# Kernel tuning notes

Hardware: AMD Instinct MI355X
Metric: run time of the kernel (lower is better)

## Reference

```python
import jax, jax.numpy as jnp
import numpy as np

DIM = 256
WH, WW = 7, 7
N = WH * WW
HEADS = 8
HEAD_DIM = DIM // HEADS
SCALE = HEAD_DIM ** -0.5
B_ = 4096
NW = 64  # windows per image; B_ % NW == 0


def _relative_position_index():
    coords = np.stack(np.meshgrid(np.arange(WH), np.arange(WW), indexing='ij'))  # (2,Wh,Ww)
    flat = coords.reshape(2, -1)  # (2,N)
    rel = flat[:, :, None] - flat[:, None, :]  # (2,N,N)
    rel = rel.transpose(1, 2, 0)  # (N,N,2)
    rel = rel + np.array([WH - 1, WW - 1])
    rel = rel * np.array([2 * WW - 1, 1])
    return rel.sum(-1).astype(np.int32)  # (N,N)


def setup_inputs() -> dict:
    key = jax.random.key(0)
    ks = jax.random.split(key, 7)
    num_rel = (2 * WH - 1) * (2 * WW - 1)
    return {
        'x': jax.random.normal(ks[0], (B_, N, DIM), jnp.float32),
        'mask': jax.random.normal(ks[1], (NW, N, N), jnp.float32),
        'qkv_w': jax.random.normal(ks[2], (DIM, 3 * DIM), jnp.float32) * 0.02,
        'qkv_b': jnp.zeros((3 * DIM,), jnp.float32),
        'proj_w': jax.random.normal(ks[3], (DIM, DIM), jnp.float32) * 0.02,
        'proj_b': jnp.zeros((DIM,), jnp.float32),
        'bias_table': jax.random.normal(ks[4], (num_rel, HEADS), jnp.float32) * 0.02,
        'rel_index': jnp.asarray(_relative_position_index()),
    }


def reference(x, mask, qkv_w, qkv_b, proj_w, proj_b, bias_table, rel_index):
    B, n, C = x.shape
    qkv = x @ qkv_w + qkv_b  # (B,N,3C)
    qkv = qkv.reshape(B, n, 3, HEADS, HEAD_DIM).transpose(2, 0, 3, 1, 4)
    q, k, v = qkv[0], qkv[1], qkv[2]  # (B,H,N,hd)
    attn = jnp.einsum('bhnd,bhmd->bhnm', q * SCALE, k)  # (B,H,N,N)
    rel_bias = bias_table[rel_index.reshape(-1)].reshape(n, n, HEADS)
    attn = attn + rel_bias.transpose(2, 0, 1)[None]  # (B,H,N,N)
    nW = mask.shape[0]
    attn = attn.reshape(-1, nW, HEADS, n, n) + mask[None, :, None]
    attn = attn.reshape(-1, HEADS, n, n)
    attn = jax.nn.softmax(attn, axis=-1)
    out = jnp.einsum('bhnm,bhmd->bhnd', attn, v)  # (B,H,N,hd)
    out = out.transpose(0, 2, 1, 3).reshape(B, n, C)
    return out @ proj_w + proj_b
```

## Files before the change

kernel.cpp:

```cpp
#include <hip/hip_runtime.h>
#include <hip/hip_bf16.h>


#define NTOK 49
static constexpr float SCALE_Q = 0.17677669529663687f;

using bf16   = __bf16;
using bf16x4 = __attribute__((ext_vector_type(4))) __bf16;
using bf16x8 = __attribute__((ext_vector_type(8))) __bf16;
using short4v = __attribute__((ext_vector_type(4))) short;
using f32x4  = __attribute__((ext_vector_type(4))) float;

#define WT_QKV_OFF 0
#define WT_PROJ_OFF (768 * 256 * 2)
#define SB_OFF (WT_PROJ_OFF + 256 * 256 * 2)
#define SM_OFF (SB_OFF + 8 * 4096 * 4)
#define WS_NEEDED (SM_OFF + (size_t)64 * 4096 * 4)

static __device__ __forceinline__ f32x4 mfma16(bf16x4 a, bf16x4 b, f32x4 c) {
#if __has_builtin(__builtin_amdgcn_mfma_f32_16x16x16_bf16)
    return __builtin_amdgcn_mfma_f32_16x16x16_bf16(a, b, c, 0, 0, 0);
#elif __has_builtin(__builtin_amdgcn_mfma_f32_16x16x16bf16_1k)
    return __builtin_amdgcn_mfma_f32_16x16x16bf16_1k(
        __builtin_bit_cast(short4v, a), __builtin_bit_cast(short4v, b), c, 0, 0, 0);
#elif __has_builtin(__builtin_amdgcn_mfma_f32_16x16x16_bf16_1k)
    return __builtin_amdgcn_mfma_f32_16x16x16_bf16_1k(
        __builtin_bit_cast(short4v, a), __builtin_bit_cast(short4v, b), c, 0, 0, 0);
#else
    asm volatile("v_mfma_f32_16x16x16_bf16 %0, %1, %2, %0\n\t"
                 "s_nop 7\n\ts_nop 7\n\ts_nop 1"
                 : "+v"(c) : "v"(a), "v"(b));
    return c;
#endif
}

__global__ void prep_wqkv(const float* __restrict__ qkv_w, bf16* __restrict__ wt) {
    int idx = blockIdx.x * 256 + threadIdx.x;
    if (idx >= 768 * 256) return;
    int n = idx >> 8, k = idx & 255;
    float v = qkv_w[k * 768 + n];
    if (n < 256) v *= SCALE_Q;
    wt[idx] = (bf16)v;
}
__global__ void prep_wproj(const float* __restrict__ proj_w, bf16* __restrict__ wt) {
    int idx = blockIdx.x * 256 + threadIdx.x;
    if (idx >= 256 * 256) return;
    int n = idx >> 8, k = idx & 255;
    wt[idx] = (bf16)proj_w[k * 256 + n];
}
__global__ void prep_sb(const float* __restrict__ bias_table, const int* __restrict__ rel_index,
                        float* __restrict__ sb) {
    int idx = blockIdx.x * 256 + threadIdx.x;
    if (idx >= 8 * 4096) return;
    int r    = idx & 3;
    int lane = (idx >> 2) & 63;
    int qp   = (idx >> 8) & 15;
    int h    = idx >> 12;
    int kt = qp >> 2, qt = qp & 3;
    int i = qt * 16 + (lane & 15);
    int j = kt * 16 + (lane >> 4) * 4 + r;
    float v;
    if (j >= NTOK)      v = -1e30f;
    else if (i >= NTOK) v = 0.0f;
    else v = bias_table[rel_index[i * 49 + j] * 8 + h];
    sb[idx] = v;
}
__global__ void prep_sm(const float* __restrict__ mask, float* __restrict__ sm) {
    int idx = blockIdx.x * 256 + threadIdx.x;
    if (idx >= 64 * 4096) return;
    int r    = idx & 3;
    int lane = (idx >> 2) & 63;
    int qp   = (idx >> 8) & 15;
    int w    = idx >> 12;
    int kt = qp >> 2, qt = qp & 3;
    int i = qt * 16 + (lane & 15);
    int j = kt * 16 + (lane >> 4) * 4 + r;
    sm[idx] = (i < NTOK && j < NTOK) ? mask[(w * 49 + i) * 49 + j] : 0.0f;
}

__global__ __launch_bounds__(256, 2) void fused_attn(
    const float* __restrict__ x,
    const float* __restrict__ qkv_b,
    const float* __restrict__ proj_b,
    const bf16* __restrict__ wt_qkv,
    const bf16* __restrict__ wt_proj,
    const float* __restrict__ sb,
    const float* __restrict__ sm,
    float* __restrict__ out)
{
    __shared__ char xs[32768];
    const int b    = blockIdx.x;
    const int tid  = threadIdx.x;
    const int lane = tid & 63;
    const int wv   = tid >> 6;
    const int c    = lane & 15;
    const int g    = lane >> 4;

    {
        const float* xb = x + (size_t)b * (NTOK * 256);
        #pragma unroll
        for (int bt = 0; bt < 2; ++bt) {
            float4 xr[8];
            #pragma unroll
            for (int it = 0; it < 8; ++it) {
                int idx = bt * 2048 + it * 256 + tid;
                int row = idx >> 6, c4 = idx & 63;
                xr[it] = make_float4(0.f, 0.f, 0.f, 0.f);
                if (row < NTOK) xr[it] = ((const float4*)xb)[row * 64 + c4];
            }
            #pragma unroll
            for (int it = 0; it < 8; ++it) {
                int idx = bt * 2048 + it * 256 + tid;
                int row = idx >> 6, c4 = idx & 63;
                bf16x4 o;
                o[0] = (bf16)xr[it].x; o[1] = (bf16)xr[it].y;
                o[2] = (bf16)xr[it].z; o[3] = (bf16)xr[it].w;
                *(bf16x4*)(xs + row * 512 + ((c4 * 8) ^ ((row & 7) << 4))) = o;
            }
        }
    }
    __syncthreads();

    bf16x4 iden;
    #pragma unroll
    for (int j = 0; j < 4; ++j) iden[j] = (bf16)((4 * g + j == c) ? 1.0f : 0.0f);

    bf16x4 ob[2][2][4];

    #pragma unroll
    for (int hh = 0; hh < 2; ++hh) {
        const int h = wv + hh * 4;

        bf16x4 qf[4][2];
        bf16x4 kf[4][2];
        bf16x4 vf[2][4];

        {
            f32x4 acc[2][4];
            #pragma unroll
            for (int ni = 0; ni < 2; ++ni)
                #pragma unroll
                for (int mi = 0; mi < 4; ++mi)
                    acc[ni][mi] = (f32x4){0.f, 0.f, 0.f, 0.f};
            #pragma unroll
            for (int kk = 0; kk < 8; ++kk) {
                bf16x8 bb[2];
                #pragma unroll
                for (int ni = 0; ni < 2; ++ni) {
                    int ncol = h * 32 + ni * 16 + c;
                    bb[ni] = *(const bf16x8*)(wt_qkv + ncol * 256 + kk * 32 + g * 8);
                }
                bf16x8 a[4];
                #pragma unroll
                for (int mi = 0; mi < 4; ++mi) {
                    int row = mi * 16 + c;
                    a[mi] = *(const bf16x8*)(xs + row * 512 + ((kk * 64 + g * 16) ^ ((row & 7) << 4)));
                }
                #pragma unroll
                for (int ni = 0; ni < 2; ++ni)
                    #pragma unroll
                    for (int mi = 0; mi < 4; ++mi)
                        acc[ni][mi] = __builtin_amdgcn_mfma_f32_16x16x32_bf16(a[mi], bb[ni], acc[ni][mi], 0, 0, 0);
            }
            #pragma unroll
            for (int ni = 0; ni < 2; ++ni) {
                float bias = qkv_b[h * 32 + ni * 16 + c] * SCALE_Q;
                #pragma unroll
                for (int mi = 0; mi < 4; ++mi) {
                    bf16x4 in;
                    #pragma unroll
                    for (int r = 0; r < 4; ++r) in[r] = (bf16)(acc[ni][mi][r] + bias);
                    f32x4 t = mfma16(in, iden, (f32x4){0.f, 0.f, 0.f, 0.f});
                    #pragma unroll
                    for (int r = 0; r < 4; ++r) qf[mi][ni][r] = (bf16)t[r];
                }
            }
        }

        {
            f32x4 acc[2][4];
            #pragma unroll
            for (int ni = 0; ni < 2; ++ni)
                #pragma unroll
                for (int mi = 0; mi < 4; ++mi)
                    acc[ni][mi] = (f32x4){0.f, 0.f, 0.f, 0.f};
            #pragma unroll
            for (int kk = 0; kk < 8; ++kk) {
                bf16x8 bb[2];
                #pragma unroll
                for (int ni = 0; ni < 2; ++ni) {
                    int ncol = 256 + h * 32 + ni * 16 + c;
                    bb[ni] = *(const bf16x8*)(wt_qkv + ncol * 256 + kk * 32 + g * 8);
                }
                bf16x8 a[4];
                #pragma unroll
                for (int mi = 0; mi < 4; ++mi) {
                    int row = mi * 16 + c;
                    a[mi] = *(const bf16x8*)(xs + row * 512 + ((kk * 64 + g * 16) ^ ((row & 7) << 4)));
                }
                #pragma unroll
                for (int ni = 0; ni < 2; ++ni)
                    #pragma unroll
                    for (int mi = 0; mi < 4; ++mi)
                        acc[ni][mi] = __builtin_amdgcn_mfma_f32_16x16x32_bf16(a[mi], bb[ni], acc[ni][mi], 0, 0, 0);
            }
            #pragma unroll
            for (int ni = 0; ni < 2; ++ni) {
                float bias = qkv_b[256 + h * 32 + ni * 16 + c];
                #pragma unroll
                for (int mi = 0; mi < 4; ++mi) {
                    bf16x4 in;
                    #pragma unroll
                    for (int r = 0; r < 4; ++r) in[r] = (bf16)(acc[ni][mi][r] + bias);
                    f32x4 t = mfma16(in, iden, (f32x4){0.f, 0.f, 0.f, 0.f});
                    #pragma unroll
                    for (int r = 0; r < 4; ++r) kf[mi][ni][r] = (bf16)t[r];
                }
            }
        }

        {
            f32x4 acc[2][4];
            #pragma unroll
            for (int dt = 0; dt < 2; ++dt)
                #pragma unroll
                for (int mi = 0; mi < 4; ++mi)
                    acc[dt][mi] = (f32x4){0.f, 0.f, 0.f, 0.f};
            #pragma unroll
            for (int kk = 0; kk < 8; ++kk) {
                bf16x8 bv[2];
                #pragma unroll
                for (int dt = 0; dt < 2; ++dt) {
                    int ncol = 512 + h * 32 + dt * 16 + c;
                    bv[dt] = *(const bf16x8*)(wt_qkv + ncol * 256 + kk * 32 + g * 8);
                }
                bf16x8 a[4];
                #pragma unroll
                for (int mi = 0; mi < 4; ++mi) {
                    int row = mi * 16 + c;
                    a[mi] = *(const bf16x8*)(xs + row * 512 + ((kk * 64 + g * 16) ^ ((row & 7) << 4)));
                }
                #pragma unroll
                for (int dt = 0; dt < 2; ++dt)
                    #pragma unroll
                    for (int mi = 0; mi < 4; ++mi)
                        acc[dt][mi] = __builtin_amdgcn_mfma_f32_16x16x32_bf16(a[mi], bv[dt], acc[dt][mi], 0, 0, 0);
            }
            #pragma unroll
            for (int dt = 0; dt < 2; ++dt) {
                float vb = qkv_b[512 + h * 32 + dt * 16 + c];
                #pragma unroll
                for (int kt = 0; kt < 4; ++kt)
                    #pragma unroll
                    for (int r = 0; r < 4; ++r) vf[dt][kt][r] = (bf16)(acc[dt][kt][r] + vb);
            }
        }

        const float* sbh = sb + (size_t)h * 4096;
        const float* smw = sm + (size_t)(b & 63) * 4096;
        #pragma unroll
        for (int qt = 0; qt < 4; ++qt) {
            f32x4 sbv[4];
            #pragma unroll
            for (int kt = 0; kt < 4; ++kt)
                sbv[kt] = *(const f32x4*)(sbh + (kt * 4 + qt) * 256 + lane * 4);

            f32x4 sT[4];
            __builtin_amdgcn_s_setprio(1);
            #pragma unroll
            for (int kt = 0; kt < 4; ++kt) {
                sT[kt] = (f32x4){0.f, 0.f, 0.f, 0.f};
                sT[kt] = mfma16(kf[kt][0], qf[qt][0], sT[kt]);
                sT[kt] = mfma16(kf[kt][1], qf[qt][1], sT[kt]);
            }
            __builtin_amdgcn_s_setprio(0);
            f32x4 smv[4];
            #pragma unroll
            for (int kt = 0; kt < 4; ++kt)
                smv[kt] = *(const f32x4*)(smw + (kt * 4 + qt) * 256 + lane * 4);
            #pragma unroll
            for (int kt = 0; kt < 4; ++kt)
                #pragma unroll
                for (int r = 0; r < 4; ++r)
                    sT[kt][r] += sbv[kt][r] + smv[kt][r];
            float m = sT[0][0];
            #pragma unroll
            for (int kt = 0; kt < 4; ++kt)
                #pragma unroll
                for (int r = 0; r < 4; ++r) m = fmaxf(m, sT[kt][r]);
            m = fmaxf(m, __shfl_xor(m, 16));
            m = fmaxf(m, __shfl_xor(m, 32));
            float sum = 0.f;
            #pragma unroll
            for (int kt = 0; kt < 4; ++kt)
                #pragma unroll
                for (int r = 0; r < 4; ++r) {
                    float e = __expf(sT[kt][r] - m);
                    sT[kt][r] = e;
                    sum += e;
                }
            sum += __shfl_xor(sum, 16);
            sum += __shfl_xor(sum, 32);
            float rs = 1.f / sum;
            bf16x4 pB[4];
            #pragma unroll
            for (int kt = 0; kt < 4; ++kt)
                #pragma unroll
                for (int r = 0; r < 4; ++r) pB[kt][r] = (bf16)(sT[kt][r] * rs);
            __builtin_amdgcn_s_setprio(1);
            #pragma unroll
            for (int dt = 0; dt < 2; ++dt) {
                f32x4 oT = (f32x4){0.f, 0.f, 0.f, 0.f};
                #pragma unroll
                for (int kt = 0; kt < 4; ++kt)
                    oT = mfma16(vf[dt][kt], pB[kt], oT);
                #pragma unroll
                for (int r = 0; r < 4; ++r) ob[hh][dt][qt][r] = (bf16)oT[r];
            }
            __builtin_amdgcn_s_setprio(0);
        }
    }
    __syncthreads();

    #pragma unroll
    for (int hh = 0; hh < 2; ++hh) {
        int h = wv + hh * 4;
        #pragma unroll
        for (int qt = 0; qt < 4; ++qt) {
            int row = qt * 16 + c;
            #pragma unroll
            for (int dt = 0; dt < 2; ++dt) {
                int cbyte = h * 64 + dt * 32 + g * 8;
                *(bf16x4*)(xs + row * 512 + (cbyte ^ ((row & 7) << 4))) = ob[hh][dt][qt];
            }
        }
    }
    __syncthreads();

    {
        f32x4 po[4][4];
        #pragma unroll
        for (int ni = 0; ni < 4; ++ni)
            #pragma unroll
            for (int mi = 0; mi < 4; ++mi)
                po[ni][mi] = (f32x4){0.f, 0.f, 0.f, 0.f};

        #pragma unroll
        for (int kk = 0; kk < 8; ++kk) {
            bf16x8 bw[4];
            #pragma unroll
            for (int ni = 0; ni < 4; ++ni) {
                int col = wv * 64 + ni * 16 + c;
                bw[ni] = *(const bf16x8*)(wt_proj + col * 256 + kk * 32 + g * 8);
            }
            bf16x8 a[4];
            #pragma unroll
            for (int mi = 0; mi < 4; ++mi) {
                int row = mi * 16 + c;
                a[mi] = *(const bf16x8*)(xs + row * 512 + ((kk * 64 + g * 16) ^ ((row & 7) << 4)));
            }
            #pragma unroll
            for (int ni = 0; ni < 4; ++ni)
                #pragma unroll
                for (int mi = 0; mi < 4; ++mi)
                    po[ni][mi] = __builtin_amdgcn_mfma_f32_16x16x32_bf16(a[mi], bw[ni], po[ni][mi], 0, 0, 0);
        }
        float* outb = out + (size_t)b * (NTOK * 256);
        #pragma unroll
        for (int ni = 0; ni < 4; ++ni) {
            int col = wv * 64 + ni * 16 + c;
            float pb = proj_b[col];
            #pragma unroll
            for (int mi = 0; mi < 4; ++mi) {
                #pragma unroll
                for (int r = 0; r < 4; ++r) {
                    int row = mi * 16 + g * 4 + r;
                    if (row < NTOK) outb[row * 256 + col] = po[ni][mi][r] + pb;
                }
            }
        }
    }
}

extern "C" void kernel_launch(void* const* d_in, const int* in_sizes, int n_in,
                              void* d_out, int out_size, void* d_ws, size_t ws_size,
                              hipStream_t stream) {
    const float* x          = (const float*)d_in[0];
    const float* mask       = (const float*)d_in[1];
    const float* qkv_w      = (const float*)d_in[2];
    const float* qkv_b      = (const float*)d_in[3];
    const float* proj_w     = (const float*)d_in[4];
    const float* proj_b     = (const float*)d_in[5];
    const float* bias_table = (const float*)d_in[6];
    const int*   rel_index  = (const int*)d_in[7];
    float* out = (float*)d_out;

    if (ws_size < WS_NEEDED) return;

    char* ws = (char*)d_ws;
    bf16*  wt_qkv  = (bf16*)(ws + WT_QKV_OFF);
    bf16*  wt_proj = (bf16*)(ws + WT_PROJ_OFF);
    float* sbp     = (float*)(ws + SB_OFF);
    float* smp     = (float*)(ws + SM_OFF);

    prep_wqkv <<<768, 256, 0, stream>>>(qkv_w, wt_qkv);
    prep_wproj<<<256, 256, 0, stream>>>(proj_w, wt_proj);
    prep_sb   <<<128, 256, 0, stream>>>(bias_table, rel_index, sbp);
    prep_sm   <<<1024, 256, 0, stream>>>(mask, smp);

    fused_attn<<<4096, 256, 0, stream>>>(x, qkv_b, proj_b, wt_qkv, wt_proj, sbp, smp, out);
}
```

Measured before the change: 374.6 us.

## Use one wave per head with 512-thread blocks and reorder V projection

The block grows from 4 to 8 waves so each wave owns a single head instead of looping over two heads, and the output projection is split into 32 columns per wave. The V projection is moved after the softmax, and the mask loads are hoisted ahead of the QK MFMAs. The GEMM k-loops are unrolled in pairs of k-steps. This is meant to raise parallelism and shorten each wave's serial chain, at the cost of more waves per CU competing under launch_bounds(512,2), which caps registers per thread.

```diff
diff --git a/kernel.cpp b/kernel.cpp
--- a/kernel.cpp
+++ b/kernel.cpp
@@ -78,7 +78,7 @@
     sm[idx] = (i < NTOK && j < NTOK) ? mask[(w * 49 + i) * 49 + j] : 0.0f;
 }
 
-__global__ __launch_bounds__(256, 2) void fused_attn(
+__global__ __launch_bounds__(512, 2) void fused_attn(
     const float* __restrict__ x,
     const float* __restrict__ qkv_b,
     const float* __restrict__ proj_b,
@@ -92,31 +92,28 @@
     const int b    = blockIdx.x;
     const int tid  = threadIdx.x;
     const int lane = tid & 63;
-    const int wv   = tid >> 6;
+    const int h    = tid >> 6;
     const int c    = lane & 15;
     const int g    = lane >> 4;
 
     {
         const float* xb = x + (size_t)b * (NTOK * 256);
-        #pragma unroll
-        for (int bt = 0; bt < 2; ++bt) {
-            float4 xr[8];
-            #pragma unroll
-            for (int it = 0; it < 8; ++it) {
-                int idx = bt * 2048 + it * 256 + tid;
-                int row = idx >> 6, c4 = idx & 63;
-                xr[it] = make_float4(0.f, 0.f, 0.f, 0.f);
-                if (row < NTOK) xr[it] = ((const float4*)xb)[row * 64 + c4];
-            }
-            #pragma unroll
-            for (int it = 0; it < 8; ++it) {
-                int idx = bt * 2048 + it * 256 + tid;
-                int row = idx >> 6, c4 = idx & 63;
-                bf16x4 o;
-                o[0] = (bf16)xr[it].x; o[1] = (bf16)xr[it].y;
-                o[2] = (bf16)xr[it].z; o[3] = (bf16)xr[it].w;
-                *(bf16x4*)(xs + row * 512 + ((c4 * 8) ^ ((row & 7) << 4))) = o;
-            }
+        float4 xr[8];
+        #pragma unroll
+        for (int it = 0; it < 8; ++it) {
+            int idx = it * 512 + tid;
+            int row = idx >> 6, c4 = idx & 63;
+            xr[it] = make_float4(0.f, 0.f, 0.f, 0.f);
+            if (row < NTOK) xr[it] = ((const float4*)xb)[row * 64 + c4];
+        }
+        #pragma unroll
+        for (int it = 0; it < 8; ++it) {
+            int idx = it * 512 + tid;
+            int row = idx >> 6, c4 = idx & 63;
+            bf16x4 o;
+            o[0] = (bf16)xr[it].x; o[1] = (bf16)xr[it].y;
+            o[2] = (bf16)xr[it].z; o[3] = (bf16)xr[it].w;
+            *(bf16x4*)(xs + row * 512 + ((c4 * 8) ^ ((row & 7) << 4))) = o;
         }
     }
     __syncthreads();
@@ -125,145 +122,120 @@
     #pragma unroll
     for (int j = 0; j < 4; ++j) iden[j] = (bf16)((4 * g + j == c) ? 1.0f : 0.0f);
 
-    bf16x4 ob[2][2][4];
-
-    #pragma unroll
-    for (int hh = 0; hh < 2; ++hh) {
-        const int h = wv + hh * 4;
-
-        bf16x4 qf[4][2];
-        bf16x4 kf[4][2];
-        bf16x4 vf[2][4];
-
-        {
-            f32x4 acc[2][4];
+    bf16x4 qf[4][2];
+    bf16x4 kf[4][2];
+    bf16x4 pB[4][4];
+    bf16x4 vf[2][4];
+    bf16x4 ob[2][4];
+
+    {
+        f32x4 acc[2][4];
+        #pragma unroll
+        for (int ni = 0; ni < 2; ++ni)
+            #pragma unroll
+            for (int mi = 0; mi < 4; ++mi)
+                acc[ni][mi] = (f32x4){0.f, 0.f, 0.f, 0.f};
+        #pragma unroll
+        for (int k2 = 0; k2 < 4; ++k2) {
+            bf16x8 bb[2][2];
             #pragma unroll
             for (int ni = 0; ni < 2; ++ni)
                 #pragma unroll
-                for (int mi = 0; mi < 4; ++mi)
-                    acc[ni][mi] = (f32x4){0.f, 0.f, 0.f, 0.f};
-            #pragma unroll
-            for (int kk = 0; kk < 8; ++kk) {
-                bf16x8 bb[2];
-                #pragma unroll
-                for (int ni = 0; ni < 2; ++ni) {
-                    int ncol = h * 32 + ni * 16 + c;
-                    bb[ni] = *(const bf16x8*)(wt_qkv + ncol * 256 + kk * 32 + g * 8);
-                }
-                bf16x8 a[4];
+                for (int hf = 0; hf < 2; ++hf)
+                    bb[ni][hf] = *(const bf16x8*)(wt_qkv + (h * 32 + ni * 16 + c) * 256
+                                                  + k2 * 64 + hf * 32 + g * 8);
+            bf16x8 a[2][4];
+            #pragma unroll
+            for (int hf = 0; hf < 2; ++hf)
                 #pragma unroll
                 for (int mi = 0; mi < 4; ++mi) {
                     int row = mi * 16 + c;
-                    a[mi] = *(const bf16x8*)(xs + row * 512 + ((kk * 64 + g * 16) ^ ((row & 7) << 4)));
-                }
+                    a[hf][mi] = *(const bf16x8*)(xs + row * 512
+                                 + ((k2 * 128 + hf * 64 + g * 16) ^ ((row & 7) << 4)));
+                }
+            #pragma unroll
+            for (int hf = 0; hf < 2; ++hf)
                 #pragma unroll
                 for (int ni = 0; ni < 2; ++ni)
                     #pragma unroll
                     for (int mi = 0; mi < 4; ++mi)
-                        acc[ni][mi] = __builtin_amdgcn_mfma_f32_16x16x32_bf16(a[mi], bb[ni], acc[ni][mi], 0, 0, 0);
+                        acc[ni][mi] = __builtin_amdgcn_mfma_f32_16x16x32_bf16(a[hf][mi], bb[ni][hf], acc[ni][mi], 0, 0, 0);
+        }
+        #pragma unroll
+        for (int ni = 0; ni < 2; ++ni) {
+            float bias = qkv_b[h * 32 + ni * 16 + c] * SCALE_Q;
+            #pragma unroll
+            for (int mi = 0; mi < 4; ++mi) {
+                bf16x4 in;
+                #pragma unroll
+                for (int r = 0; r < 4; ++r) in[r] = (bf16)(acc[ni][mi][r] + bias);
+                f32x4 t = mfma16(in, iden, (f32x4){0.f, 0.f, 0.f, 0.f});
+                #pragma unroll
+                for (int r = 0; r < 4; ++r) qf[mi][ni][r] = (bf16)t[r];
             }
-            #pragma unroll
-            for (int ni = 0; ni < 2; ++ni) {
-                float bias = qkv_b[h * 32 + ni * 16 + c] * SCALE_Q;
-                #pragma unroll
-                for (int mi = 0; mi < 4; ++mi) {
-                    bf16x4 in;
-                    #pragma unroll
-                    for (int r = 0; r < 4; ++r) in[r] = (bf16)(acc[ni][mi][r] + bias);
-                    f32x4 t = mfma16(in, iden, (f32x4){0.f, 0.f, 0.f, 0.f});
-                    #pragma unroll
-                    for (int r = 0; r < 4; ++r) qf[mi][ni][r] = (bf16)t[r];
-                }
-            }
-        }
-
-        {
-            f32x4 acc[2][4];
+        }
+    }
+
+    {
+        f32x4 acc[2][4];
+        #pragma unroll
+        for (int ni = 0; ni < 2; ++ni)
+            #pragma unroll
+            for (int mi = 0; mi < 4; ++mi)
+                acc[ni][mi] = (f32x4){0.f, 0.f, 0.f, 0.f};
+        #pragma unroll
+        for (int k2 = 0; k2 < 4; ++k2) {
+            bf16x8 bb[2][2];
             #pragma unroll
             for (int ni = 0; ni < 2; ++ni)
                 #pragma unroll
-                for (int mi = 0; mi < 4; ++mi)
-                    acc[ni][mi] = (f32x4){0.f, 0.f, 0.f, 0.f};
-            #pragma unroll
-            for (int kk = 0; kk < 8; ++kk) {
-                bf16x8 bb[2];
-                #pragma unroll
-                for (int ni = 0; ni < 2; ++ni) {
-                    int ncol = 256 + h * 32 + ni * 16 + c;
-                    bb[ni] = *(const bf16x8*)(wt_qkv + ncol * 256 + kk * 32 + g * 8);
-                }
-                bf16x8 a[4];
+                for (int hf = 0; hf < 2; ++hf)
+                    bb[ni][hf] = *(const bf16x8*)(wt_qkv + (256 + h * 32 + ni * 16 + c) * 256
+                                                  + k2 * 64 + hf * 32 + g * 8);
+            bf16x8 a[2][4];
+            #pragma unroll
+            for (int hf = 0; hf < 2; ++hf)
                 #pragma unroll
                 for (int mi = 0; mi < 4; ++mi) {
                     int row = mi * 16 + c;
-                    a[mi] = *(const bf16x8*)(xs + row * 512 + ((kk * 64 + g * 16) ^ ((row & 7) << 4)));
-                }
+                    a[hf][mi] = *(const bf16x8*)(xs + row * 512
+                                 + ((k2 * 128 + hf * 64 + g * 16) ^ ((row & 7) << 4)));
+                }
+            #pragma unroll
+            for (int hf = 0; hf < 2; ++hf)
                 #pragma unroll
                 for (int ni = 0; ni < 2; ++ni)
                     #pragma unroll
                     for (int mi = 0; mi < 4; ++mi)
-                        acc[ni][mi] = __builtin_amdgcn_mfma_f32_16x16x32_bf16(a[mi], bb[ni], acc[ni][mi], 0, 0, 0);
+                        acc[ni][mi] = __builtin_amdgcn_mfma_f32_16x16x32_bf16(a[hf][mi], bb[ni][hf], acc[ni][mi], 0, 0, 0);
+        }
+        #pragma unroll
+        for (int ni = 0; ni < 2; ++ni) {
+            float bias = qkv_b[256 + h * 32 + ni * 16 + c];
+            #pragma unroll
+            for (int mi = 0; mi < 4; ++mi) {
+                bf16x4 in;
+                #pragma unroll
+                for (int r = 0; r < 4; ++r) in[r] = (bf16)(acc[ni][mi][r] + bias);
+                f32x4 t = mfma16(in, iden, (f32x4){0.f, 0.f, 0.f, 0.f});
+                #pragma unroll
+                for (int r = 0; r < 4; ++r) kf[mi][ni][r] = (bf16)t[r];
             }
-            #pragma unroll
-            for (int ni = 0; ni < 2; ++ni) {
-                float bias = qkv_b[256 + h * 32 + ni * 16 + c];
-                #pragma unroll
-                for (int mi = 0; mi < 4; ++mi) {
-                    bf16x4 in;
-                    #pragma unroll
-                    for (int r = 0; r < 4; ++r) in[r] = (bf16)(acc[ni][mi][r] + bias);
-                    f32x4 t = mfma16(in, iden, (f32x4){0.f, 0.f, 0.f, 0.f});
-                    #pragma unroll
-                    for (int r = 0; r < 4; ++r) kf[mi][ni][r] = (bf16)t[r];
-                }
-            }
-        }
-
-        {
-            f32x4 acc[2][4];
-            #pragma unroll
-            for (int dt = 0; dt < 2; ++dt)
-                #pragma unroll
-                for (int mi = 0; mi < 4; ++mi)
-                    acc[dt][mi] = (f32x4){0.f, 0.f, 0.f, 0.f};
-            #pragma unroll
-            for (int kk = 0; kk < 8; ++kk) {
-                bf16x8 bv[2];
-                #pragma unroll
-                for (int dt = 0; dt < 2; ++dt) {
-                    int ncol = 512 + h * 32 + dt * 16 + c;
-                    bv[dt] = *(const bf16x8*)(wt_qkv + ncol * 256 + kk * 32 + g * 8);
-                }
-                bf16x8 a[4];
-                #pragma unroll
-                for (int mi = 0; mi < 4; ++mi) {
-                    int row = mi * 16 + c;
-                    a[mi] = *(const bf16x8*)(xs + row * 512 + ((kk * 64 + g * 16) ^ ((row & 7) << 4)));
-                }
-                #pragma unroll
-                for (int dt = 0; dt < 2; ++dt)
-                    #pragma unroll
-                    for (int mi = 0; mi < 4; ++mi)
-                        acc[dt][mi] = __builtin_amdgcn_mfma_f32_16x16x32_bf16(a[mi], bv[dt], acc[dt][mi], 0, 0, 0);
-            }
-            #pragma unroll
-            for (int dt = 0; dt < 2; ++dt) {
-                float vb = qkv_b[512 + h * 32 + dt * 16 + c];
-                #pragma unroll
-                for (int kt = 0; kt < 4; ++kt)
-                    #pragma unroll
-                    for (int r = 0; r < 4; ++r) vf[dt][kt][r] = (bf16)(acc[dt][kt][r] + vb);
-            }
-        }
-
+        }
+    }
+
+    {
         const float* sbh = sb + (size_t)h * 4096;
         const float* smw = sm + (size_t)(b & 63) * 4096;
         #pragma unroll
         for (int qt = 0; qt < 4; ++qt) {
-            f32x4 sbv[4];
+            f32x4 sbv[4], smv[4];
             #pragma unroll
             for (int kt = 0; kt < 4; ++kt)
                 sbv[kt] = *(const f32x4*)(sbh + (kt * 4 + qt) * 256 + lane * 4);
+            #pragma unroll
+            for (int kt = 0; kt < 4; ++kt)
+                smv[kt] = *(const f32x4*)(smw + (kt * 4 + qt) * 256 + lane * 4);
 
             f32x4 sT[4];
             __builtin_amdgcn_s_setprio(1);
@@ -274,10 +246,6 @@
                 sT[kt] = mfma16(kf[kt][1], qf[qt][1], sT[kt]);
             }
             __builtin_amdgcn_s_setprio(0);
-            f32x4 smv[4];
-            #pragma unroll
-            for (int kt = 0; kt < 4; ++kt)
-                smv[kt] = *(const f32x4*)(smw + (kt * 4 + qt) * 256 + lane * 4);
             #pragma unroll
             for (int kt = 0; kt < 4; ++kt)
                 #pragma unroll
@@ -302,73 +270,121 @@
             sum += __shfl_xor(sum, 16);
             sum += __shfl_xor(sum, 32);
             float rs = 1.f / sum;
-            bf16x4 pB[4];
-            #pragma unroll
-            for (int kt = 0; kt < 4; ++kt)
-                #pragma unroll
-                for (int r = 0; r < 4; ++r) pB[kt][r] = (bf16)(sT[kt][r] * rs);
-            __builtin_amdgcn_s_setprio(1);
-            #pragma unroll
-            for (int dt = 0; dt < 2; ++dt) {
-                f32x4 oT = (f32x4){0.f, 0.f, 0.f, 0.f};
-                #pragma unroll
-                for (int kt = 0; kt < 4; ++kt)
-                    oT = mfma16(vf[dt][kt], pB[kt], oT);
-                #pragma unroll
-                for (int r = 0; r < 4; ++r) ob[hh][dt][qt][r] = (bf16)oT[r];
-            }
-            __builtin_amdgcn_s_setprio(0);
-        }
-    }
+            #pragma unroll
+            for (int kt = 0; kt < 4; ++kt)
+                #pragma unroll
+                for (int r = 0; r < 4; ++r) pB[qt][kt][r] = (bf16)(sT[kt][r] * rs);
+        }
+    }
+
+    {
+        f32x4 acc[2][4];
+        #pragma unroll
+        for (int dt = 0; dt < 2; ++dt)
+            #pragma unroll
+            for (int mi = 0; mi < 4; ++mi)
+                acc[dt][mi] = (f32x4){0.f, 0.f, 0.f, 0.f};
+        #pragma unroll
+        for (int k2 = 0; k2 < 4; ++k2) {
+            bf16x8 bb[2][2];
+            #pragma unroll
+            for (int dt = 0; dt < 2; ++dt)
+                #pragma unroll
+                for (int hf = 0; hf < 2; ++hf)
+                    bb[dt][hf] = *(const bf16x8*)(wt_qkv + (512 + h * 32 + dt * 16 + c) * 256
+                                                  + k2 * 64 + hf * 32 + g * 8);
+            bf16x8 a[2][4];
+            #pragma unroll
+            for (int hf = 0; hf < 2; ++hf)
+                #pragma unroll
+                for (int mi = 0; mi < 4; ++mi) {
+                    int row = mi * 16 + c;
+                    a[hf][mi] = *(const bf16x8*)(xs + row * 512
+                                 + ((k2 * 128 + hf * 64 + g * 16) ^ ((row & 7) << 4)));
+                }
+            #pragma unroll
+            for (int hf = 0; hf < 2; ++hf)
+                #pragma unroll
+                for (int dt = 0; dt < 2; ++dt)
+                    #pragma unroll
+                    for (int mi = 0; mi < 4; ++mi)
+                        acc[dt][mi] = __builtin_amdgcn_mfma_f32_16x16x32_bf16(a[hf][mi], bb[dt][hf], acc[dt][mi], 0, 0, 0);
+        }
+        #pragma unroll
+        for (int dt = 0; dt < 2; ++dt) {
+            float vb = qkv_b[512 + h * 32 + dt * 16 + c];
+            #pragma unroll
+            for (int kt = 0; kt < 4; ++kt)
+                #pragma unroll
+                for (int r = 0; r < 4; ++r) vf[dt][kt][r] = (bf16)(acc[dt][kt][r] + vb);
+        }
+    }
+
+    __builtin_amdgcn_s_setprio(1);
+    #pragma unroll
+    for (int qt = 0; qt < 4; ++qt) {
+        #pragma unroll
+        for (int dt = 0; dt < 2; ++dt) {
+            f32x4 oT = (f32x4){0.f, 0.f, 0.f, 0.f};
+            #pragma unroll
+            for (int kt = 0; kt < 4; ++kt)
+                oT = mfma16(vf[dt][kt], pB[qt][kt], oT);
+            #pragma unroll
+            for (int r = 0; r < 4; ++r) ob[dt][qt][r] = (bf16)oT[r];
+        }
+    }
+    __builtin_amdgcn_s_setprio(0);
     __syncthreads();
 
     #pragma unroll
-    for (int hh = 0; hh < 2; ++hh) {
-        int h = wv + hh * 4;
-        #pragma unroll
-        for (int qt = 0; qt < 4; ++qt) {
-            int row = qt * 16 + c;
-            #pragma unroll
-            for (int dt = 0; dt < 2; ++dt) {
-                int cbyte = h * 64 + dt * 32 + g * 8;
-                *(bf16x4*)(xs + row * 512 + (cbyte ^ ((row & 7) << 4))) = ob[hh][dt][qt];
-            }
+    for (int qt = 0; qt < 4; ++qt) {
+        int row = qt * 16 + c;
+        #pragma unroll
+        for (int dt = 0; dt < 2; ++dt) {
+            int cbyte = h * 64 + dt * 32 + g * 8;
+            *(bf16x4*)(xs + row * 512 + (cbyte ^ ((row & 7) << 4))) = ob[dt][qt];
         }
     }
     __syncthreads();
 
     {
-        f32x4 po[4][4];
-        #pragma unroll
-        for (int ni = 0; ni < 4; ++ni)
+        f32x4 po[2][4];
+        #pragma unroll
+        for (int ni = 0; ni < 2; ++ni)
             #pragma unroll
             for (int mi = 0; mi < 4; ++mi)
                 po[ni][mi] = (f32x4){0.f, 0.f, 0.f, 0.f};
 
         #pragma unroll
-        for (int kk = 0; kk < 8; ++kk) {
-            bf16x8 bw[4];
-            #pragma unroll
-            for (int ni = 0; ni < 4; ++ni) {
-                int col = wv * 64 + ni * 16 + c;
-                bw[ni] = *(const bf16x8*)(wt_proj + col * 256 + kk * 32 + g * 8);
-            }
-            bf16x8 a[4];
-            #pragma unroll
-            for (int mi = 0; mi < 4; ++mi) {
-                int row = mi * 16 + c;
-                a[mi] = *(const bf16x8*)(xs + row * 512 + ((kk * 64 + g * 16) ^ ((row & 7) << 4)));
-            }
-            #pragma unroll
-            for (int ni = 0; ni < 4; ++ni)
-                #pragma unroll
-                for (int mi = 0; mi < 4; ++mi)
-                    po[ni][mi] = __builtin_amdgcn_mfma_f32_16x16x32_bf16(a[mi], bw[ni], po[ni][mi], 0, 0, 0);
+        for (int k2 = 0; k2 < 4; ++k2) {
+            bf16x8 bw[2][2];
+            #pragma unroll
+            for (int ni = 0; ni < 2; ++ni)
+                #pragma unroll
+                for (int hf = 0; hf < 2; ++hf)
+                    bw[ni][hf] = *(const bf16x8*)(wt_proj + (h * 32 + ni * 16 + c) * 256
+                                                  + k2 * 64 + hf * 32 + g * 8);
+            bf16x8 a[2][4];
+            #pragma unroll
+            for (int hf = 0; hf < 2; ++hf)
+                #pragma unroll
+                for (int mi = 0; mi < 4; ++mi) {
+                    int row = mi * 16 + c;
+                    a[hf][mi] = *(const bf16x8*)(xs + row * 512
+                                 + ((k2 * 128 + hf * 64 + g * 16) ^ ((row & 7) << 4)));
+                }
+            #pragma unroll
+            for (int hf = 0; hf < 2; ++hf)
+                #pragma unroll
+                for (int ni = 0; ni < 2; ++ni)
+                    #pragma unroll
+                    for (int mi = 0; mi < 4; ++mi)
+                        po[ni][mi] = __builtin_amdgcn_mfma_f32_16x16x32_bf16(a[hf][mi], bw[ni][hf], po[ni][mi], 0, 0, 0);
         }
         float* outb = out + (size_t)b * (NTOK * 256);
         #pragma unroll
-        for (int ni = 0; ni < 4; ++ni) {
-            int col = wv * 64 + ni * 16 + c;
+        for (int ni = 0; ni < 2; ++ni) {
+            int col = h * 32 + ni * 16 + c;
             float pb = proj_b[col];
             #pragma unroll
             for (int mi = 0; mi < 4; ++mi) {
@@ -408,5 +424,5 @@
     prep_sb   <<<128, 256, 0, stream>>>(bias_table, rel_index, sbp);
     prep_sm   <<<1024, 256, 0, stream>>>(mask, smp);
 
-    fused_attn<<<4096, 256, 0, stream>>>(x, qkv_b, proj_b, wt_qkv, wt_proj, sbp, smp, out);
-}
+    fused_attn<<<4096, 512, 0, stream>>>(x, qkv_b, proj_b, wt_qkv, wt_proj, sbp, smp, out);
+}
```

New measurement: 373.0 us. About the same (-0.4%).
